# Performance work log

Hardware: AMD Instinct MI355X
Metric: run time of the kernel (lower is better)

## Reference

```python
import jax, jax.numpy as jnp
import numpy as np

EPS = 1e-5
NEG_INF = -1e30


def layer_norm_seq(x, gamma, beta):
    # Faithful to the custom LayerNorm: normalizes over dim=1 (the T axis of
    # [B, T, C]) with UNBIASED variance (torch.var default), then scales by
    # gamma/beta of shape [C] broadcast over the last axis.
    m = jnp.mean(x, axis=1, keepdims=True)
    v = jnp.var(x, axis=1, keepdims=True, ddof=1)
    return gamma * (x - m) / jnp.sqrt(v + EPS) + beta


def setup_inputs() -> dict:
    key = jax.random.key(0)
    B, T, C, H = 4, 1024, 1024, 16
    hd = C // H  # 64
    ks = jax.random.split(key, 10)
    s_in = 1.0 / np.sqrt(C)
    s_ff = 1.0 / np.sqrt(4 * C)
    return {
        "x": jax.random.normal(ks[0], (B, T, C), dtype=jnp.float32),
        # NOTE: Head uses self.key(x) for BOTH q and k; the query Linear is
        # dead code, so only key/value weights are materialized.
        "Wk": jax.random.uniform(ks[1], (H, C, hd), minval=-s_in, maxval=s_in, dtype=jnp.float32),
        "Wv": jax.random.uniform(ks[2], (H, C, hd), minval=-s_in, maxval=s_in, dtype=jnp.float32),
        "Wp": jax.random.uniform(ks[3], (C, C), minval=-s_in, maxval=s_in, dtype=jnp.float32),
        "bp": jnp.zeros((C,), dtype=jnp.float32),
        "W1": jax.random.uniform(ks[4], (4 * C, C), minval=-s_in, maxval=s_in, dtype=jnp.float32),
        "b1": jnp.zeros((4 * C,), dtype=jnp.float32),
        "W2": jax.random.uniform(ks[5], (C, 4 * C), minval=-s_ff, maxval=s_ff, dtype=jnp.float32),
        "b2": jnp.zeros((C,), dtype=jnp.float32),
        "g1": jnp.ones((C,), dtype=jnp.float32),
        "beta1": jnp.zeros((C,), dtype=jnp.float32),
        "g2": jnp.ones((C,), dtype=jnp.float32),
        "beta2": jnp.zeros((C,), dtype=jnp.float32),
    }


def reference(x, Wk, Wv, Wp, bp, W1, b1, W2, b2, g1, beta1, g2, beta2):
    B, T, C = x.shape
    H, _, hd = Wk.shape
    scale = hd ** -0.5

    # --- self-attention sublayer (pre-LN over sequence axis) ---
    h = layer_norm_seq(x, g1, beta1)
    # q and k BOTH use the key projection (faithful to the original bug).
    qk = jnp.einsum("btc,hcd->bhtd", h, Wk)          # [B,H,T,hd]
    v = jnp.einsum("btc,hcd->bhtd", h, Wv)           # [B,H,T,hd]
    wei = jnp.einsum("bhtd,bhsd->bhts", qk, qk) * scale  # [B,H,T,T]
    causal = jnp.tril(jnp.ones((T, T), dtype=bool))
    wei = jnp.where(causal, wei, NEG_INF)
    wei = jax.nn.softmax(wei, axis=-1)
    attn = jnp.einsum("bhts,bhsd->bthd", wei, v).reshape(B, T, C)
    attn = attn @ Wp.T + bp
    x = x + attn

    # --- feed-forward sublayer ---
    h2 = layer_norm_seq(x, g2, beta2)
    ff = jax.nn.relu(h2 @ W1.T + b1) @ W2.T + b2
    return x + ff
```

## Files before the change

kernel.cpp:

```cpp
#include <hip/hip_runtime.h>
#include <stdint.h>


#define BDIM 256

typedef __attribute__((ext_vector_type(8))) __bf16 bf16x8;
typedef __attribute__((ext_vector_type(4))) float f32x4;

__device__ __forceinline__ unsigned short f2bf(float f) {
    unsigned u = __float_as_uint(f);
    u += 0x7fff + ((u >> 16) & 1);
    return (unsigned short)(u >> 16);
}

__device__ __forceinline__ void gload_lds16(const void* g, void* l) {
    __builtin_amdgcn_global_load_lds(
        (const __attribute__((address_space(1))) void*)g,
        (__attribute__((address_space(3))) void*)l, 16, 0, 0);
}

__global__ void k_cast_bf16(const float* __restrict__ in, unsigned short* __restrict__ out, int n4) {
    int i = blockIdx.x * BDIM + threadIdx.x;
    if (i >= n4) return;
    float4 v = ((const float4*)in)[i];
    ushort4 o;
    o.x = f2bf(v.x); o.y = f2bf(v.y); o.z = f2bf(v.z); o.w = f2bf(v.w);
    ((ushort4*)out)[i] = o;
}

__global__ void k_headT(const float* __restrict__ W, unsigned short* __restrict__ out) {
    __shared__ float tile[64][65];
    const int tid = threadIdx.x;
    const int c0 = blockIdx.x * 64, h = blockIdx.y;
    const float* src = W + ((long)h << 16) + (long)c0 * 64;
    #pragma unroll
    for (int j = 0; j < 16; ++j) {
        int idx = j * 256 + tid;
        tile[idx >> 6][idx & 63] = src[idx];
    }
    __syncthreads();
    #pragma unroll
    for (int j = 0; j < 16; ++j) {
        int idx = j * 256 + tid;
        int d = idx >> 6, c = idx & 63;
        out[(long)(h * 64 + d) * 1024 + c0 + c] = f2bf(tile[c][d]);
    }
}

__global__ void k_ln_part(const float* __restrict__ x, float* __restrict__ psum, float* __restrict__ psq) {
    int c = blockIdx.x * BDIM + threadIdx.x;
    int tc = blockIdx.y, b = blockIdx.z;
    const float* p = x + ((long)b << 20) + ((long)tc * 128) * 1024 + c;
    float s = 0.f, ss = 0.f;
    for (int t = 0; t < 128; ++t) {
        float v = p[t * 1024];
        s += v; ss += v * v;
    }
    int o = (b * 8 + tc) * 1024 + c;
    psum[o] = s; psq[o] = ss;
}

__global__ void k_ln_fin(const float* __restrict__ psum, const float* __restrict__ psq,
                         float* __restrict__ mean, float* __restrict__ rstd) {
    int i = blockIdx.x * BDIM + threadIdx.x;
    int b = i >> 10, c = i & 1023;
    float s = 0.f, ss = 0.f;
    for (int j = 0; j < 8; ++j) {
        s  += psum[(b * 8 + j) * 1024 + c];
        ss += psq[(b * 8 + j) * 1024 + c];
    }
    float m = s * (1.0f / 1024.0f);
    float var = (ss - 1024.0f * m * m) * (1.0f / 1023.0f);
    mean[i] = m;
    rstd[i] = rsqrtf(var + 1e-5f);
}

__global__ void k_ln_apply(const float* __restrict__ x, const float* __restrict__ mean,
                           const float* __restrict__ rstd, const float* __restrict__ g,
                           const float* __restrict__ beta, unsigned short* __restrict__ out) {
    int i = blockIdx.x * BDIM + threadIdx.x;
    int flat = i << 2;
    int b = flat >> 20, c = flat & 1023;
    float4 xv = ((const float4*)x)[i];
    float4 mv = *(const float4*)&mean[(b << 10) + c];
    float4 rv = *(const float4*)&rstd[(b << 10) + c];
    float4 gv = *(const float4*)&g[c];
    float4 bv = *(const float4*)&beta[c];
    ushort4 o;
    o.x = f2bf(gv.x * (xv.x - mv.x) * rv.x + bv.x);
    o.y = f2bf(gv.y * (xv.y - mv.y) * rv.y + bv.y);
    o.z = f2bf(gv.z * (xv.z - mv.z) * rv.z + bv.z);
    o.w = f2bf(gv.w * (xv.w - mv.w) * rv.w + bv.w);
    ((ushort4*)out)[i] = o;
}

template <int EPI>
__global__ __launch_bounds__(256, 2) void k_gemm_bt(
    const unsigned short* __restrict__ A, const unsigned short* __restrict__ B,
    void* __restrict__ Cv, const float* __restrict__ bias, const float* __restrict__ res,
    int N, int K, long sA, long sB, long sC)
{
    __shared__ __align__(16) unsigned short As[128 * 32];
    __shared__ __align__(16) unsigned short Bs[128 * 32];
    const int tid = threadIdx.x;
    const int wave = tid >> 6, lane = tid & 63;
    const long bz = blockIdx.z;
    const int m0 = blockIdx.y * 128, n0 = blockIdx.x * 128;
    const unsigned short* Ab = A + bz * sA;
    const unsigned short* Bb = B + bz * sB;

    const int srow = wave * 16 + (lane >> 2);
    const int skel = (lane & 3) * 8;
    const unsigned short* gA0 = Ab + (long)(m0 + srow) * K + skel;
    const unsigned short* gB0 = Bb + (long)(n0 + srow) * K + skel;
    unsigned short* lA0 = As + wave * 512;
    unsigned short* lA1 = As + 2048 + wave * 512;
    unsigned short* lB0 = Bs + wave * 512;
    unsigned short* lB1 = Bs + 2048 + wave * 512;
    const long rowoff = (long)64 * K;

    f32x4 acc[4][4] = {};

    const int wm = (wave >> 1) * 64, wn = (wave & 1) * 64;
    const int lr = lane & 15, lg = lane >> 4;
    const int aoff = lg * 8;

    for (int kt = 0; kt < K; kt += 32) {
        __syncthreads();
        gload_lds16(gA0 + kt, lA0);
        gload_lds16(gA0 + rowoff + kt, lA1);
        gload_lds16(gB0 + kt, lB0);
        gload_lds16(gB0 + rowoff + kt, lB1);
        __syncthreads();
        bf16x8 af[4], bfr[4];
        #pragma unroll
        for (int i = 0; i < 4; ++i) {
            af[i]  = *(const bf16x8*)&As[(wm + i * 16 + lr) * 32 + aoff];
            bfr[i] = *(const bf16x8*)&Bs[(wn + i * 16 + lr) * 32 + aoff];
        }
        #pragma unroll
        for (int i = 0; i < 4; ++i)
            #pragma unroll
            for (int j = 0; j < 4; ++j)
                acc[i][j] = __builtin_amdgcn_mfma_f32_16x16x32_bf16(af[i], bfr[j], acc[i][j], 0, 0, 0);
    }

    const int cr0 = lg * 4;
    #pragma unroll
    for (int mi = 0; mi < 4; ++mi) {
        #pragma unroll
        for (int r = 0; r < 4; ++r) {
            const int row = m0 + wm + mi * 16 + cr0 + r;
            const long rb = bz * sC + (long)row * N;
            #pragma unroll
            for (int nj = 0; nj < 4; ++nj) {
                const int col = n0 + wn + nj * 16 + lr;
                float v = acc[mi][nj][r];
                if (EPI == 0) {
                    ((unsigned short*)Cv)[rb + col] = f2bf(v);
                } else if (EPI == 1) {
                    ((float*)Cv)[rb + col] = v + bias[col] + res[rb + col];
                } else {
                    v += bias[col];
                    ((unsigned short*)Cv)[rb + col] = f2bf(v > 0.f ? v : 0.f);
                }
            }
        }
    }
}

#define CEXP 0.18033688f
#define PSTRIDE 72

__global__ __launch_bounds__(256, 2) void k_attn(
    const unsigned short* __restrict__ qk, const unsigned short* __restrict__ vt,
    unsigned short* __restrict__ ctx)
{
    __shared__ __align__(16) unsigned short Ks[64 * 64];
    __shared__ __align__(16) unsigned short Vs[64 * 64];
    __shared__ __align__(16) unsigned short P[4][16 * PSTRIDE];
    const int tid = threadIdx.x;
    const int wave = tid >> 6, lane = tid & 63;
    const int bh = blockIdx.x >> 3, pairIdx = blockIdx.x & 7;
    const int b = bh >> 4, h = bh & 15;
    const int lr = lane & 15, lg = lane >> 4;

    const int swz = (lr & 7) << 4;
    const int cby0 = (lg * 16) ^ swz;
    const int cby1 = (64 + lg * 16) ^ swz;
    const int srow_l = lane >> 3;
    const int scol = ((lane & 7) * 8) ^ (srow_l << 3);

    unsigned short* Pw = P[wave];
    char* KsB = (char*)Ks;
    char* VsB = (char*)Vs;
    const unsigned short* qbase = qk + ((long)b << 20) + h * 64;
    const unsigned short* vb    = vt + ((long)(b * 16 + h) << 16);

    #pragma unroll 1
    for (int phase = 0; phase < 2; ++phase) {
        const int qb = phase ? (15 - pairIdx) : pairIdx;
        const int q0 = qb << 6;
        const int qw = q0 + wave * 16;

        const unsigned short* qrow = qbase + (long)(qw + lr) * 1024 + lg * 8;
        const bf16x8 aq0 = *(const bf16x8*)qrow;
        const bf16x8 aq1 = *(const bf16x8*)(qrow + 32);

        f32x4 acc[4] = {};
        float mrow[4] = {-1e30f, -1e30f, -1e30f, -1e30f};
        float lrow[4] = {0.f, 0.f, 0.f, 0.f};

        for (int c = 0; c <= qb; ++c) {
            const int k0 = c << 6;
            __syncthreads();
            #pragma unroll
            for (int i = 0; i < 2; ++i) {
                const int row = i * 32 + wave * 8 + srow_l;
                gload_lds16(qbase + (long)(k0 + row) * 1024 + scol,
                            KsB + i * 4096 + wave * 1024);
                gload_lds16(vb + (long)row * 1024 + k0 + scol,
                            VsB + i * 4096 + wave * 1024);
            }
            __syncthreads();

            f32x4 s[4];
            #pragma unroll
            for (int t = 0; t < 4; ++t) {
                const int r = t * 16 + lr;
                bf16x8 bk0 = *(const bf16x8*)(KsB + r * 128 + cby0);
                bf16x8 bk1 = *(const bf16x8*)(KsB + r * 128 + cby1);
                f32x4 z = {};
                z = __builtin_amdgcn_mfma_f32_16x16x32_bf16(aq0, bk0, z, 0, 0, 0);
                s[t] = __builtin_amdgcn_mfma_f32_16x16x32_bf16(aq1, bk1, z, 0, 0, 0);
            }
            if (c == qb) {
                #pragma unroll
                for (int t = 0; t < 4; ++t) {
                    const int col = t * 16 + lr;
                    #pragma unroll
                    for (int r = 0; r < 4; ++r)
                        if (col > wave * 16 + lg * 4 + r) s[t][r] = -1e30f;
                }
            }
            float fac[4];
            #pragma unroll
            for (int r = 0; r < 4; ++r) {
                float v = fmaxf(fmaxf(s[0][r], s[1][r]), fmaxf(s[2][r], s[3][r]));
                v = fmaxf(v, __shfl_xor(v, 1));
                v = fmaxf(v, __shfl_xor(v, 2));
                v = fmaxf(v, __shfl_xor(v, 4));
                v = fmaxf(v, __shfl_xor(v, 8));
                float mn = fmaxf(mrow[r], v);
                fac[r] = exp2f((mrow[r] - mn) * CEXP);
                mrow[r] = mn;
            }
            float psum[4] = {0.f, 0.f, 0.f, 0.f};
            #pragma unroll
            for (int t = 0; t < 4; ++t) {
                #pragma unroll
                for (int r = 0; r < 4; ++r) {
                    float p = exp2f((s[t][r] - mrow[r]) * CEXP);
                    psum[r] += p;
                    Pw[(lg * 4 + r) * PSTRIDE + t * 16 + lr] = f2bf(p);
                }
            }
            #pragma unroll
            for (int r = 0; r < 4; ++r) {
                float v = psum[r];
                v += __shfl_xor(v, 1); v += __shfl_xor(v, 2);
                v += __shfl_xor(v, 4); v += __shfl_xor(v, 8);
                lrow[r] = lrow[r] * fac[r] + v;
            }
            #pragma unroll
            for (int ni = 0; ni < 4; ++ni)
                #pragma unroll
                for (int r = 0; r < 4; ++r)
                    acc[ni][r] *= fac[r];
            const bf16x8 pa0 = *(const bf16x8*)&Pw[lr * PSTRIDE + lg * 8];
            const bf16x8 pa1 = *(const bf16x8*)&Pw[lr * PSTRIDE + 32 + lg * 8];
            #pragma unroll
            for (int ni = 0; ni < 4; ++ni) {
                const int vr = ni * 16 + lr;
                bf16x8 bv0 = *(const bf16x8*)(VsB + vr * 128 + cby0);
                bf16x8 bv1 = *(const bf16x8*)(VsB + vr * 128 + cby1);
                acc[ni] = __builtin_amdgcn_mfma_f32_16x16x32_bf16(pa0, bv0, acc[ni], 0, 0, 0);
                acc[ni] = __builtin_amdgcn_mfma_f32_16x16x32_bf16(pa1, bv1, acc[ni], 0, 0, 0);
            }
        }

        unsigned short* crow = ctx + ((long)(b * 1024 + qw)) * 1024 + h * 64;
        #pragma unroll
        for (int r = 0; r < 4; ++r) {
            const float inv = 1.0f / lrow[r];
            #pragma unroll
            for (int ni = 0; ni < 4; ++ni)
                crow[(long)(lg * 4 + r) * 1024 + ni * 16 + lr] = f2bf(acc[ni][r] * inv);
        }
    }
}

extern "C" void kernel_launch(void* const* d_in, const int* in_sizes, int n_in,
                              void* d_out, int out_size, void* d_ws, size_t ws_size,
                              hipStream_t stream)
{
    const float* x   = (const float*)d_in[0];
    const float* Wk  = (const float*)d_in[1];
    const float* Wv  = (const float*)d_in[2];
    const float* Wp  = (const float*)d_in[3];
    const float* bp  = (const float*)d_in[4];
    const float* W1  = (const float*)d_in[5];
    const float* b1  = (const float*)d_in[6];
    const float* W2  = (const float*)d_in[7];
    const float* b2  = (const float*)d_in[8];
    const float* g1  = (const float*)d_in[9];
    const float* be1 = (const float*)d_in[10];
    const float* g2  = (const float*)d_in[11];
    const float* be2 = (const float*)d_in[12];
    float* out = (float*)d_out;

    char* ws = (char*)d_ws;
    const long MB = 1024 * 1024;
    unsigned short* BkT = (unsigned short*)(ws);
    unsigned short* WvT = (unsigned short*)(ws + 2 * MB);
    unsigned short* WpB = (unsigned short*)(ws + 4 * MB);
    unsigned short* W1B = (unsigned short*)(ws + 6 * MB);
    unsigned short* W2B = (unsigned short*)(ws + 14 * MB);
    unsigned short* hB  = (unsigned short*)(ws + 22 * MB);
    unsigned short* qkB = (unsigned short*)(ws + 30 * MB);
    unsigned short* VtB = (unsigned short*)(ws + 38 * MB);
    unsigned short* ctx = (unsigned short*)(ws + 46 * MB);
    unsigned short* ff1 = (unsigned short*)(ws + 30 * MB);
    float* x2   = (float*)(ws + 62 * MB);
    float* psum = (float*)(ws + 78 * MB);
    float* psq  = (float*)(ws + 78 * MB + 128 * 1024);
    float* mean = (float*)(ws + 78 * MB + 256 * 1024);
    float* rstd = (float*)(ws + 78 * MB + 272 * 1024);

    k_cast_bf16<<<1024, BDIM, 0, stream>>>(Wp, WpB, 262144);
    k_cast_bf16<<<4096, BDIM, 0, stream>>>(W1, W1B, 1048576);
    k_cast_bf16<<<4096, BDIM, 0, stream>>>(W2, W2B, 1048576);
    k_headT<<<dim3(16, 16), BDIM, 0, stream>>>(Wk, BkT);
    k_headT<<<dim3(16, 16), BDIM, 0, stream>>>(Wv, WvT);

    k_ln_part<<<dim3(4, 8, 4), BDIM, 0, stream>>>(x, psum, psq);
    k_ln_fin<<<16, BDIM, 0, stream>>>(psum, psq, mean, rstd);
    k_ln_apply<<<4096, BDIM, 0, stream>>>(x, mean, rstd, g1, be1, hB);

    k_gemm_bt<0><<<dim3(8, 32, 1), BDIM, 0, stream>>>(hB, BkT, qkB, nullptr, nullptr, 1024, 1024, 0, 0, 0);
    k_gemm_bt<0><<<dim3(8, 8, 4), BDIM, 0, stream>>>(WvT, hB, VtB, nullptr, nullptr, 1024, 1024, 0, MB, MB);

    k_attn<<<512, BDIM, 0, stream>>>(qkB, VtB, ctx);

    k_gemm_bt<1><<<dim3(8, 32, 1), BDIM, 0, stream>>>(ctx, WpB, x2, bp, x, 1024, 1024, 0, 0, 0);

    k_ln_part<<<dim3(4, 8, 4), BDIM, 0, stream>>>(x2, psum, psq);
    k_ln_fin<<<16, BDIM, 0, stream>>>(psum, psq, mean, rstd);
    k_ln_apply<<<4096, BDIM, 0, stream>>>(x2, mean, rstd, g2, be2, hB);

    k_gemm_bt<2><<<dim3(32, 32, 1), BDIM, 0, stream>>>(hB, W1B, ff1, b1, nullptr, 4096, 1024, 0, 0, 0);
    k_gemm_bt<1><<<dim3(8, 32, 1), BDIM, 0, stream>>>(ff1, W2B, out, b2, x2, 1024, 4096, 0, 0, 0);
}
```

Baseline: 394.8 us.

## Double-buffer GEMM LDS tiles and split-K the FFN down-projection with atomics

The GEMM kernel now double-buffers its A/B LDS tiles, prefetching the next K-slice with direct global-to-LDS loads while the MFMAs run on the current one, and uses one barrier per iteration instead of two. Occupancy hint rises to 3 blocks per CU. The K=4096 second FFN GEMM is split into two K-halves that atomically add into an output pre-initialised with residual plus bias by a new elementwise kernel. This raises parallelism for that GEMM, at the cost of doubled LDS per block, float atomics with nondeterministic summation order, and an extra pass over the output.

```diff
diff --git a/kernel.cpp b/kernel.cpp
--- a/kernel.cpp
+++ b/kernel.cpp
@@ -94,14 +94,24 @@
     ((ushort4*)out)[i] = o;
 }
 
+__global__ void k_addbias(const float* __restrict__ res, const float* __restrict__ bias,
+                          float* __restrict__ out) {
+    int i = blockIdx.x * BDIM + threadIdx.x;
+    int c = (i << 2) & 1023;
+    float4 r = ((const float4*)res)[i];
+    float4 bv = *(const float4*)&bias[c];
+    r.x += bv.x; r.y += bv.y; r.z += bv.z; r.w += bv.w;
+    ((float4*)out)[i] = r;
+}
+
 template <int EPI>
-__global__ __launch_bounds__(256, 2) void k_gemm_bt(
+__global__ __launch_bounds__(256, 3) void k_gemm_bt(
     const unsigned short* __restrict__ A, const unsigned short* __restrict__ B,
     void* __restrict__ Cv, const float* __restrict__ bias, const float* __restrict__ res,
-    int N, int K, long sA, long sB, long sC)
+    int N, int K, int ldA, int ldB, long sA, long sB, long sC)
 {
-    __shared__ __align__(16) unsigned short As[128 * 32];
-    __shared__ __align__(16) unsigned short Bs[128 * 32];
+    __shared__ __align__(16) unsigned short As[2][128 * 32];
+    __shared__ __align__(16) unsigned short Bs[2][128 * 32];
     const int tid = threadIdx.x;
     const int wave = tid >> 6, lane = tid & 63;
     const long bz = blockIdx.z;
@@ -111,13 +121,11 @@
 
     const int srow = wave * 16 + (lane >> 2);
     const int skel = (lane & 3) * 8;
-    const unsigned short* gA0 = Ab + (long)(m0 + srow) * K + skel;
-    const unsigned short* gB0 = Bb + (long)(n0 + srow) * K + skel;
-    unsigned short* lA0 = As + wave * 512;
-    unsigned short* lA1 = As + 2048 + wave * 512;
-    unsigned short* lB0 = Bs + wave * 512;
-    unsigned short* lB1 = Bs + 2048 + wave * 512;
-    const long rowoff = (long)64 * K;
+    const unsigned short* gA0 = Ab + (long)(m0 + srow) * ldA + skel;
+    const unsigned short* gB0 = Bb + (long)(n0 + srow) * ldB + skel;
+    const long rowoffA = (long)64 * ldA;
+    const long rowoffB = (long)64 * ldB;
+    const int lofs = wave * 512;
 
     f32x4 acc[4][4] = {};
 
@@ -125,24 +133,38 @@
     const int lr = lane & 15, lg = lane >> 4;
     const int aoff = lg * 8;
 
+    gload_lds16(gA0, &As[0][lofs]);
+    gload_lds16(gA0 + rowoffA, &As[0][2048 + lofs]);
+    gload_lds16(gB0, &Bs[0][lofs]);
+    gload_lds16(gB0 + rowoffB, &Bs[0][2048 + lofs]);
+    asm volatile("s_waitcnt vmcnt(0)" ::: "memory");
+    __builtin_amdgcn_s_barrier();
+    __builtin_amdgcn_sched_barrier(0);
+
+    int cur = 0;
     for (int kt = 0; kt < K; kt += 32) {
-        __syncthreads();
-        gload_lds16(gA0 + kt, lA0);
-        gload_lds16(gA0 + rowoff + kt, lA1);
-        gload_lds16(gB0 + kt, lB0);
-        gload_lds16(gB0 + rowoff + kt, lB1);
-        __syncthreads();
+        const int nxt = cur ^ 1;
+        if (kt + 32 < K) {
+            gload_lds16(gA0 + kt + 32, &As[nxt][lofs]);
+            gload_lds16(gA0 + rowoffA + kt + 32, &As[nxt][2048 + lofs]);
+            gload_lds16(gB0 + kt + 32, &Bs[nxt][lofs]);
+            gload_lds16(gB0 + rowoffB + kt + 32, &Bs[nxt][2048 + lofs]);
+        }
         bf16x8 af[4], bfr[4];
         #pragma unroll
         for (int i = 0; i < 4; ++i) {
-            af[i]  = *(const bf16x8*)&As[(wm + i * 16 + lr) * 32 + aoff];
-            bfr[i] = *(const bf16x8*)&Bs[(wn + i * 16 + lr) * 32 + aoff];
+            af[i]  = *(const bf16x8*)&As[cur][(wm + i * 16 + lr) * 32 + aoff];
+            bfr[i] = *(const bf16x8*)&Bs[cur][(wn + i * 16 + lr) * 32 + aoff];
         }
         #pragma unroll
         for (int i = 0; i < 4; ++i)
             #pragma unroll
             for (int j = 0; j < 4; ++j)
                 acc[i][j] = __builtin_amdgcn_mfma_f32_16x16x32_bf16(af[i], bfr[j], acc[i][j], 0, 0, 0);
+        asm volatile("s_waitcnt vmcnt(0)" ::: "memory");
+        __builtin_amdgcn_s_barrier();
+        __builtin_amdgcn_sched_barrier(0);
+        cur = nxt;
     }
 
     const int cr0 = lg * 4;
@@ -160,9 +182,11 @@
                     ((unsigned short*)Cv)[rb + col] = f2bf(v);
                 } else if (EPI == 1) {
                     ((float*)Cv)[rb + col] = v + bias[col] + res[rb + col];
-                } else {
+                } else if (EPI == 2) {
                     v += bias[col];
                     ((unsigned short*)Cv)[rb + col] = f2bf(v > 0.f ? v : 0.f);
+                } else {
+                    atomicAdd(&((float*)Cv)[rb + col], v);
                 }
             }
         }
@@ -347,17 +371,19 @@
     k_ln_fin<<<16, BDIM, 0, stream>>>(psum, psq, mean, rstd);
     k_ln_apply<<<4096, BDIM, 0, stream>>>(x, mean, rstd, g1, be1, hB);
 
-    k_gemm_bt<0><<<dim3(8, 32, 1), BDIM, 0, stream>>>(hB, BkT, qkB, nullptr, nullptr, 1024, 1024, 0, 0, 0);
-    k_gemm_bt<0><<<dim3(8, 8, 4), BDIM, 0, stream>>>(WvT, hB, VtB, nullptr, nullptr, 1024, 1024, 0, MB, MB);
+    k_gemm_bt<0><<<dim3(8, 32, 1), BDIM, 0, stream>>>(hB, BkT, qkB, nullptr, nullptr, 1024, 1024, 1024, 1024, 0, 0, 0);
+    k_gemm_bt<0><<<dim3(8, 8, 4), BDIM, 0, stream>>>(WvT, hB, VtB, nullptr, nullptr, 1024, 1024, 1024, 1024, 0, MB, MB);
 
     k_attn<<<512, BDIM, 0, stream>>>(qkB, VtB, ctx);
 
-    k_gemm_bt<1><<<dim3(8, 32, 1), BDIM, 0, stream>>>(ctx, WpB, x2, bp, x, 1024, 1024, 0, 0, 0);
+    k_gemm_bt<1><<<dim3(8, 32, 1), BDIM, 0, stream>>>(ctx, WpB, x2, bp, x, 1024, 1024, 1024, 1024, 0, 0, 0);
 
     k_ln_part<<<dim3(4, 8, 4), BDIM, 0, stream>>>(x2, psum, psq);
     k_ln_fin<<<16, BDIM, 0, stream>>>(psum, psq, mean, rstd);
     k_ln_apply<<<4096, BDIM, 0, stream>>>(x2, mean, rstd, g2, be2, hB);
 
-    k_gemm_bt<2><<<dim3(32, 32, 1), BDIM, 0, stream>>>(hB, W1B, ff1, b1, nullptr, 4096, 1024, 0, 0, 0);
-    k_gemm_bt<1><<<dim3(8, 32, 1), BDIM, 0, stream>>>(ff1, W2B, out, b2, x2, 1024, 4096, 0, 0, 0);
-}
+    k_gemm_bt<2><<<dim3(32, 32, 1), BDIM, 0, stream>>>(hB, W1B, ff1, b1, nullptr, 4096, 1024, 1024, 1024, 0, 0, 0);
+
+    k_addbias<<<4096, BDIM, 0, stream>>>(x2, b2, out);
+    k_gemm_bt<3><<<dim3(8, 32, 2), BDIM, 0, stream>>>(ff1, W2B, out, nullptr, nullptr, 1024, 2048, 4096, 4096, 2048, 2048, 0);
+}
```

Result: faster. 384.1 us (-2.7%).
